# Performance work log

Measured on AMD Instinct MI355X. Metric: run time of the kernel, lower is better.

## Reference

```python
import jax, jax.numpy as jnp
import numpy as np

B, S, D = 4, 2048, 1024
P = 2
N_FEAT = 16          # n_feature_know
N_REST = 16          # n_restore_know
R = 128              # knowledge_rank
D_SPACE = 64


def setup_inputs() -> dict:
    key = jax.random.key(0)
    ks = jax.random.split(key, 6)
    x = jax.random.normal(ks[0], (B, S, D), dtype=jnp.float32)
    # per-token routing weights for each of P feature paths, in [0,1)
    feature_paths = jax.random.uniform(ks[1], (P, B, S, N_FEAT), dtype=jnp.float32)
    f_know = jax.random.normal(ks[2], (N_FEAT, D, R), dtype=jnp.float32) * 0.02
    r_know = jax.random.normal(ks[3], (N_REST, R, D), dtype=jnp.float32) * 0.02
    feature_emb = jax.random.normal(ks[4], (N_FEAT, D_SPACE), dtype=jnp.float32)
    W_router = jax.random.normal(ks[5], (D_SPACE + R, N_REST), dtype=jnp.float32) * 0.05
    return {"x": x, "feature_paths": feature_paths, "f_know": f_know,
            "r_know": r_know, "feature_emb": feature_emb, "W_router": W_router}


def reference(x, feature_paths, f_know, r_know, feature_emb, W_router):
    # Feature projection into all N low-rank banks: [B,S,N,R]
    all_h = jnp.einsum('bsd,ndr->bsnr', x, f_know)
    # Weighted sum over banks per path: [P,B,S,R]
    h_all = jnp.einsum('bsnr,pbsn->pbsr', all_h, feature_paths)
    # Context for restore routing: [P,B,S,D_SPACE]
    neuron_ctx = jnp.einsum('pbsn,nd->pbsd', feature_paths, feature_emb)
    # restore_input = cat([neuron_ctx, h]) -> router -> softmax restore weights
    restore_input = jnp.concatenate([neuron_ctx, h_all], axis=-1)  # [P,B,S,D_SPACE+R]
    logits = jnp.einsum('pbsc,cn->pbsn', restore_input, W_router)
    w = jax.nn.softmax(logits, axis=-1)                            # [P,B,S,N_REST]
    # Restore + per-token weighted combine, summed over P paths: [B,S,D]
    output = jnp.einsum('pbsr,nrd,pbsn->bsd', h_all, r_know, w)
    restore_aux_loss = jnp.float32(0.0)
    return output, restore_aux_loss
```

## Files before the change

kernel.cpp:

```cpp
#include <hip/hip_runtime.h>

typedef __attribute__((ext_vector_type(4))) float f32x4;
typedef __bf16 bf16x8 __attribute__((ext_vector_type(8)));
typedef unsigned short ushort_t;

#define T_TOK 8192
#define DIM   1024
#define NRCOL 2048

#define VMW(n)  asm volatile("s_waitcnt vmcnt(" #n ")" ::: "memory")
#define SB0()   __builtin_amdgcn_sched_barrier(0)
#define BAR()   __builtin_amdgcn_s_barrier()

static __device__ __forceinline__ unsigned short f2bf(float f) {
  unsigned int u = __builtin_bit_cast(unsigned int, f);
  u += 0x7fffu + ((u >> 16) & 1u);
  return (unsigned short)(u >> 16);
}
static __device__ __forceinline__ float bfbits2f(unsigned int lo16) {
  return __builtin_bit_cast(float, lo16 << 16);
}
static __device__ __forceinline__ void gload16(const void* g, void* l) {
  __builtin_amdgcn_global_load_lds((const __attribute__((address_space(1))) void*)g,
                                   (__attribute__((address_space(3))) void*)l, 16, 0, 0);
}

__global__ __launch_bounds__(256) void prep_kernel(const float* __restrict__ x,
                                                   const float* __restrict__ fk,
                                                   const float* __restrict__ rk,
                                                   unsigned short* __restrict__ Xbf,
                                                   unsigned short* __restrict__ W1t,
                                                   unsigned short* __restrict__ W2t) {
  const int bid = blockIdx.x, tid = threadIdx.x;
  if (bid < 2048) {
    const float4* in4 = (const float4*)x;
    uint2* o4 = (uint2*)Xbf;
    #pragma unroll
    for (int it = 0; it < 4; ++it) {
      const int i = bid * 256 + tid + it * 524288;
      float4 v = in4[i];
      uint2 o;
      o.x = (unsigned)f2bf(v.x) | ((unsigned)f2bf(v.y) << 16);
      o.y = (unsigned)f2bf(v.z) | ((unsigned)f2bf(v.w) << 16);
      o4[i] = o;
    }
    return;
  }
  __shared__ float tile[32][33];
  const float* src;
  unsigned short* dst;
  int rows, cols, r0, c0;
  if (bid < 4096) {
    const int b = bid - 2048;
    const int z = b >> 7, rem = b & 127;
    src = fk + (size_t)z * 1024 * 128;
    dst = W1t + (size_t)z * 128 * 1024;
    rows = 1024; cols = 128;
    c0 = (rem & 3) * 32; r0 = (rem >> 2) * 32;
  } else {
    const int b = bid - 4096;
    src = rk; dst = W2t;
    rows = 2048; cols = 1024;
    c0 = (b & 31) * 32; r0 = (b >> 5) * 32;
  }
  const int tx = tid & 31, ty = tid >> 5;
  #pragma unroll
  for (int i = 0; i < 32; i += 8)
    tile[ty + i][tx] = src[(size_t)(r0 + ty + i) * cols + c0 + tx];
  __syncthreads();
  #pragma unroll
  for (int i = 0; i < 32; i += 8)
    dst[(size_t)(c0 + ty + i) * rows + r0 + tx] = f2bf(tile[tx][ty + i]);
}

template<int BM, int BN, int K, bool OUT_BF16>
__global__ __launch_bounds__(256, 1) void gemmW(const ushort_t* __restrict__ A,
                                                const ushort_t* __restrict__ Bt,
                                                void* __restrict__ Cp, int N) {
  constexpr int nt = K / 64;
  constexpr int MF = BM / 32;
  constexpr int NF = BN / 32;
  constexpr int AR = BM / 32;
  constexpr int BR = BN / 32;
  __shared__ ushort_t As[3][BM * 64];
  __shared__ ushort_t Bs[3][BN * 64];

  const int tid = threadIdx.x;
  const int nx = gridDim.x;
  const int orig = blockIdx.y * nx + blockIdx.x;
  const int q = (nx * gridDim.y) >> 3;
  const int swz = (orig & 7) * q + (orig >> 3);
  const int bx = swz % nx, by = swz / nx;

  const int lane = tid & 63, wv = tid >> 6;
  const int wm = wv >> 1, wn = wv & 1;
  const int lrow = lane & 15, lk = lane >> 4;

  const ushort_t* Ab = A + (size_t)by * BM * K;
  const ushort_t* Bb = Bt + (size_t)bx * BN * K;

  const int srow = tid >> 3;
  const int sch = (tid & 7) ^ (srow & 7);
  const ushort_t* pA[AR];
  const ushort_t* pB[BR];
  #pragma unroll
  for (int r = 0; r < AR; ++r) pA[r] = Ab + (size_t)(r * 32 + srow) * K + sch * 8;
  #pragma unroll
  for (int r = 0; r < BR; ++r) pB[r] = Bb + (size_t)(r * 32 + srow) * K + sch * 8;
  const int dL = tid * 8;

  auto stage = [&](int s, int adv) {
    #pragma unroll
    for (int r = 0; r < AR; ++r) gload16(pA[r] + adv, (void*)&As[s][r * 2048 + dL]);
    #pragma unroll
    for (int r = 0; r < BR; ++r) gload16(pB[r] + adv, (void*)&Bs[s][r * 2048 + dL]);
  };

  int oA[MF], oB[NF];
  #pragma unroll
  for (int m = 0; m < MF; ++m) {
    const int r = wm * (BM / 2) + m * 16 + lrow;
    oA[m] = r * 64 + (lk ^ (r & 7)) * 8;
  }
  #pragma unroll
  for (int n = 0; n < NF; ++n) {
    const int r = wn * (BN / 2) + n * 16 + lrow;
    oB[n] = r * 64 + (lk ^ (r & 7)) * 8;
  }

  f32x4 acc[MF][NF];
  #pragma unroll
  for (int m = 0; m < MF; ++m)
    #pragma unroll
    for (int n = 0; n < NF; ++n)
      acc[m][n] = (f32x4){0.f, 0.f, 0.f, 0.f};

  stage(0, 0);
  stage(1, 64);
  VMW(12); SB0(); BAR(); SB0();

  #pragma unroll
  for (int t = 0; t < nt; ++t) {
    const int s = t % 3, s2 = (t + 2) % 3;
    if (t + 2 < nt) stage(s2, (t + 2) * 64);
    #pragma unroll
    for (int ks = 0; ks < 2; ++ks) {
      bf16x8 av[MF], bv[NF];
      #pragma unroll
      for (int m = 0; m < MF; ++m) av[m] = *(const bf16x8*)&As[s][oA[m] ^ (ks * 32)];
      #pragma unroll
      for (int n = 0; n < NF; ++n) bv[n] = *(const bf16x8*)&Bs[s][oB[n] ^ (ks * 32)];
      __builtin_amdgcn_s_setprio(1);
      #pragma unroll
      for (int m = 0; m < MF; ++m)
        #pragma unroll
        for (int n = 0; n < NF; ++n)
          acc[m][n] = __builtin_amdgcn_mfma_f32_16x16x32_bf16(av[m], bv[n], acc[m][n], 0, 0, 0);
      __builtin_amdgcn_s_setprio(0);
    }
    SB0();
    if (t + 2 < nt) { VMW(12); } else { VMW(0); }
    SB0(); BAR(); SB0();
  }

  #pragma unroll
  for (int m = 0; m < MF; ++m) {
    const int row0 = by * BM + wm * (BM / 2) + m * 16 + lk * 4;
    #pragma unroll
    for (int n = 0; n < NF; ++n) {
      const int col = bx * BN + wn * (BN / 2) + n * 16 + lrow;
      #pragma unroll
      for (int j = 0; j < 4; ++j) {
        const size_t idx = (size_t)(row0 + j) * N + col;
        if constexpr (OUT_BF16) ((ushort_t*)Cp)[idx] = f2bf(acc[m][n][j]);
        else                    ((float*)Cp)[idx] = acc[m][n][j];
      }
    }
  }
}

__global__ __launch_bounds__(256) void middle_kernel(const unsigned short* __restrict__ AH,
                                                     const float* __restrict__ fp,
                                                     const float* __restrict__ femb,
                                                     const float* __restrict__ Wr,
                                                     unsigned short* __restrict__ Mout,
                                                     float* __restrict__ auxout) {
  __shared__ float G[16][16];
  __shared__ float hs[4][2][128];
  __shared__ float wsm[4][2][16];
  const int tid = threadIdx.x;
  {
    const int n = tid >> 4, j = tid & 15;
    float s = 0.f;
    #pragma unroll
    for (int ds = 0; ds < 64; ++ds) s += femb[n * 64 + ds] * Wr[ds * 16 + j];
    G[n][j] = s;
  }
  const int wv = tid >> 6, l = tid & 63;
  const int t = blockIdx.x * 4 + wv;

  float p0[16], p1[16];
  #pragma unroll
  for (int n = 0; n < 16; ++n) {
    p0[n] = fp[t * 16 + n];
    p1[n] = fp[T_TOK * 16 + t * 16 + n];
  }

  float h00 = 0.f, h01 = 0.f, h10 = 0.f, h11 = 0.f;
  const unsigned short* ahrow = AH + (size_t)t * NRCOL;
  #pragma unroll
  for (int n = 0; n < 16; ++n) {
    const unsigned int v = *(const unsigned int*)(ahrow + n * 128 + 2 * l);
    const float a0 = bfbits2f(v & 0xffffu);
    const float a1 = bfbits2f(v >> 16);
    h00 += a0 * p0[n]; h01 += a1 * p0[n];
    h10 += a0 * p1[n]; h11 += a1 * p1[n];
  }
  hs[wv][0][2 * l] = h00; hs[wv][0][2 * l + 1] = h01;
  hs[wv][1][2 * l] = h10; hs[wv][1][2 * l + 1] = h11;
  __syncthreads();

  if (l < 32) {
    const int p = l >> 4, j = l & 15;
    float s = 0.f;
    #pragma unroll
    for (int n = 0; n < 16; ++n) s += (p ? p1[n] : p0[n]) * G[n][j];
    const float* hp = hs[wv][p];
    const float* wr = Wr + 64 * 16 + j;
    float s0 = 0.f, s1 = 0.f, s2 = 0.f, s3 = 0.f;
    #pragma unroll
    for (int r = 0; r < 128; r += 4) {
      s0 += hp[r]     * wr[(r)     * 16];
      s1 += hp[r + 1] * wr[(r + 1) * 16];
      s2 += hp[r + 2] * wr[(r + 2) * 16];
      s3 += hp[r + 3] * wr[(r + 3) * 16];
    }
    s += (s0 + s1) + (s2 + s3);
    float mx = s;
    #pragma unroll
    for (int d = 1; d < 16; d <<= 1) mx = fmaxf(mx, __shfl_xor(mx, d, 64));
    const float e = __expf(s - mx);
    float sum = e;
    #pragma unroll
    for (int d = 1; d < 16; d <<= 1) sum += __shfl_xor(sum, d, 64);
    wsm[wv][p][j] = e / sum;
  }
  __syncthreads();

  unsigned short* mrow = Mout + (size_t)t * NRCOL;
  #pragma unroll
  for (int n = 0; n < 16; ++n) {
    const float w0 = wsm[wv][0][n], w1 = wsm[wv][1][n];
    const float m0 = w0 * h00 + w1 * h10;
    const float m1 = w0 * h01 + w1 * h11;
    const unsigned int pk = (unsigned)f2bf(m0) | ((unsigned)f2bf(m1) << 16);
    *(unsigned int*)(mrow + n * 128 + 2 * l) = pk;
  }
  if (blockIdx.x == 0 && tid == 0) auxout[0] = 0.f;
}

extern "C" void kernel_launch(void* const* d_in, const int* in_sizes, int n_in,
                              void* d_out, int out_size, void* d_ws, size_t ws_size,
                              hipStream_t stream) {
  const float* x    = (const float*)d_in[0];
  const float* fp   = (const float*)d_in[1];
  const float* fk   = (const float*)d_in[2];
  const float* rk   = (const float*)d_in[3];
  const float* femb = (const float*)d_in[4];
  const float* Wr   = (const float*)d_in[5];
  float* out = (float*)d_out;

  char* ws = (char*)d_ws;
  unsigned short* Xbf = (unsigned short*)ws;
  unsigned short* W1t = (unsigned short*)(ws + 16u * 1024 * 1024);
  unsigned short* Mb  = (unsigned short*)ws;
  unsigned short* W2t = (unsigned short*)(ws + 32u * 1024 * 1024);
  unsigned short* AH  = (unsigned short*)(ws + 36u * 1024 * 1024);

  prep_kernel<<<6144, 256, 0, stream>>>(x, fk, rk, Xbf, W1t, W2t);
  gemmW<256, 128, 1024, true><<<dim3(NRCOL / 128, T_TOK / 256), 256, 0, stream>>>(Xbf, W1t, AH, NRCOL);
  middle_kernel<<<T_TOK / 4, 256, 0, stream>>>(AH, fp, femb, Wr, Mb, out + 8388608);
  gemmW<128, 256, 2048, false><<<dim3(DIM / 256, T_TOK / 128), 256, 0, stream>>>(Mb, W2t, out, DIM);
}
```

Before: 127.2 us.

## Use 128x128 double-buffered GEMM tiles with 2 blocks/CU; parallelize router dot

Replaces the templated triple-buffered GEMM, which used 256x128 or 128x256 tiles at one block per CU, with a fixed 128x128 tile, double-buffered kernel launched at two blocks per CU. This roughly doubles the grid and allows more resident waves to hide memory latency, at the cost of less operand reuse per tile and a shallower prefetch pipeline. The middle kernel now stages the router weight slice in shared memory and splits the 128-long router dot product across all 64 lanes with a shuffle reduction, instead of leaving half the lanes idle.

```diff
diff --git a/kernel.cpp b/kernel.cpp
--- a/kernel.cpp
+++ b/kernel.cpp
@@ -73,17 +73,13 @@
     dst[(size_t)(c0 + ty + i) * rows + r0 + tx] = f2bf(tile[tx][ty + i]);
 }
 
-template<int BM, int BN, int K, bool OUT_BF16>
-__global__ __launch_bounds__(256, 1) void gemmW(const ushort_t* __restrict__ A,
+template<int K, bool OUT_BF16>
+__global__ __launch_bounds__(256, 2) void gemmD(const ushort_t* __restrict__ A,
                                                 const ushort_t* __restrict__ Bt,
                                                 void* __restrict__ Cp, int N) {
   constexpr int nt = K / 64;
-  constexpr int MF = BM / 32;
-  constexpr int NF = BN / 32;
-  constexpr int AR = BM / 32;
-  constexpr int BR = BN / 32;
-  __shared__ ushort_t As[3][BM * 64];
-  __shared__ ushort_t Bs[3][BN * 64];
+  __shared__ ushort_t As[2][128 * 64];
+  __shared__ ushort_t Bs[2][128 * 64];
 
   const int tid = threadIdx.x;
   const int nx = gridDim.x;
@@ -96,79 +92,79 @@
   const int wm = wv >> 1, wn = wv & 1;
   const int lrow = lane & 15, lk = lane >> 4;
 
-  const ushort_t* Ab = A + (size_t)by * BM * K;
-  const ushort_t* Bb = Bt + (size_t)bx * BN * K;
+  const ushort_t* Ab = A + (size_t)by * 128 * K;
+  const ushort_t* Bb = Bt + (size_t)bx * 128 * K;
 
   const int srow = tid >> 3;
   const int sch = (tid & 7) ^ (srow & 7);
-  const ushort_t* pA[AR];
-  const ushort_t* pB[BR];
-  #pragma unroll
-  for (int r = 0; r < AR; ++r) pA[r] = Ab + (size_t)(r * 32 + srow) * K + sch * 8;
-  #pragma unroll
-  for (int r = 0; r < BR; ++r) pB[r] = Bb + (size_t)(r * 32 + srow) * K + sch * 8;
+  const ushort_t* pA[4];
+  const ushort_t* pB[4];
+  #pragma unroll
+  for (int r = 0; r < 4; ++r) {
+    pA[r] = Ab + (size_t)(r * 32 + srow) * K + sch * 8;
+    pB[r] = Bb + (size_t)(r * 32 + srow) * K + sch * 8;
+  }
   const int dL = tid * 8;
 
   auto stage = [&](int s, int adv) {
     #pragma unroll
-    for (int r = 0; r < AR; ++r) gload16(pA[r] + adv, (void*)&As[s][r * 2048 + dL]);
-    #pragma unroll
-    for (int r = 0; r < BR; ++r) gload16(pB[r] + adv, (void*)&Bs[s][r * 2048 + dL]);
+    for (int r = 0; r < 4; ++r) gload16(pA[r] + adv, (void*)&As[s][r * 2048 + dL]);
+    #pragma unroll
+    for (int r = 0; r < 4; ++r) gload16(pB[r] + adv, (void*)&Bs[s][r * 2048 + dL]);
   };
 
-  int oA[MF], oB[NF];
-  #pragma unroll
-  for (int m = 0; m < MF; ++m) {
-    const int r = wm * (BM / 2) + m * 16 + lrow;
+  int oA[4], oB[4];
+  #pragma unroll
+  for (int m = 0; m < 4; ++m) {
+    const int r = wm * 64 + m * 16 + lrow;
     oA[m] = r * 64 + (lk ^ (r & 7)) * 8;
   }
   #pragma unroll
-  for (int n = 0; n < NF; ++n) {
-    const int r = wn * (BN / 2) + n * 16 + lrow;
+  for (int n = 0; n < 4; ++n) {
+    const int r = wn * 64 + n * 16 + lrow;
     oB[n] = r * 64 + (lk ^ (r & 7)) * 8;
   }
 
-  f32x4 acc[MF][NF];
-  #pragma unroll
-  for (int m = 0; m < MF; ++m)
-    #pragma unroll
-    for (int n = 0; n < NF; ++n)
+  f32x4 acc[4][4];
+  #pragma unroll
+  for (int m = 0; m < 4; ++m)
+    #pragma unroll
+    for (int n = 0; n < 4; ++n)
       acc[m][n] = (f32x4){0.f, 0.f, 0.f, 0.f};
 
   stage(0, 0);
-  stage(1, 64);
-  VMW(12); SB0(); BAR(); SB0();
+  VMW(0); SB0(); BAR(); SB0();
 
   #pragma unroll
   for (int t = 0; t < nt; ++t) {
-    const int s = t % 3, s2 = (t + 2) % 3;
-    if (t + 2 < nt) stage(s2, (t + 2) * 64);
+    const int s = t & 1;
+    if (t + 1 < nt) stage(s ^ 1, (t + 1) * 64);
     #pragma unroll
     for (int ks = 0; ks < 2; ++ks) {
-      bf16x8 av[MF], bv[NF];
-      #pragma unroll
-      for (int m = 0; m < MF; ++m) av[m] = *(const bf16x8*)&As[s][oA[m] ^ (ks * 32)];
-      #pragma unroll
-      for (int n = 0; n < NF; ++n) bv[n] = *(const bf16x8*)&Bs[s][oB[n] ^ (ks * 32)];
+      bf16x8 av[4], bv[4];
+      #pragma unroll
+      for (int m = 0; m < 4; ++m) av[m] = *(const bf16x8*)&As[s][oA[m] ^ (ks * 32)];
+      #pragma unroll
+      for (int n = 0; n < 4; ++n) bv[n] = *(const bf16x8*)&Bs[s][oB[n] ^ (ks * 32)];
       __builtin_amdgcn_s_setprio(1);
       #pragma unroll
-      for (int m = 0; m < MF; ++m)
+      for (int m = 0; m < 4; ++m)
         #pragma unroll
-        for (int n = 0; n < NF; ++n)
+        for (int n = 0; n < 4; ++n)
           acc[m][n] = __builtin_amdgcn_mfma_f32_16x16x32_bf16(av[m], bv[n], acc[m][n], 0, 0, 0);
       __builtin_amdgcn_s_setprio(0);
     }
     SB0();
-    if (t + 2 < nt) { VMW(12); } else { VMW(0); }
-    SB0(); BAR(); SB0();
-  }
-
-  #pragma unroll
-  for (int m = 0; m < MF; ++m) {
-    const int row0 = by * BM + wm * (BM / 2) + m * 16 + lk * 4;
-    #pragma unroll
-    for (int n = 0; n < NF; ++n) {
-      const int col = bx * BN + wn * (BN / 2) + n * 16 + lrow;
+    if (t + 1 < nt) VMW(0);
+    BAR(); SB0();
+  }
+
+  #pragma unroll
+  for (int m = 0; m < 4; ++m) {
+    const int row0 = by * 128 + wm * 64 + m * 16 + lk * 4;
+    #pragma unroll
+    for (int n = 0; n < 4; ++n) {
+      const int col = bx * 128 + wn * 64 + n * 16 + lrow;
       #pragma unroll
       for (int j = 0; j < 4; ++j) {
         const size_t idx = (size_t)(row0 + j) * N + col;
@@ -186,6 +182,7 @@
                                                      unsigned short* __restrict__ Mout,
                                                      float* __restrict__ auxout) {
   __shared__ float G[16][16];
+  __shared__ float WrBs[128 * 16];
   __shared__ float hs[4][2][128];
   __shared__ float wsm[4][2][16];
   const int tid = threadIdx.x;
@@ -195,6 +192,9 @@
     #pragma unroll
     for (int ds = 0; ds < 64; ++ds) s += femb[n * 64 + ds] * Wr[ds * 16 + j];
     G[n][j] = s;
+    #pragma unroll
+    for (int k = 0; k < 8; ++k)
+      WrBs[tid * 8 + k] = Wr[64 * 16 + tid * 8 + k];
   }
   const int wv = tid >> 6, l = tid & 63;
   const int t = blockIdx.x * 4 + wv;
@@ -220,22 +220,25 @@
   hs[wv][1][2 * l] = h10; hs[wv][1][2 * l + 1] = h11;
   __syncthreads();
 
-  if (l < 32) {
-    const int p = l >> 4, j = l & 15;
-    float s = 0.f;
-    #pragma unroll
-    for (int n = 0; n < 16; ++n) s += (p ? p1[n] : p0[n]) * G[n][j];
-    const float* hp = hs[wv][p];
-    const float* wr = Wr + 64 * 16 + j;
+  {
+    const int p = l >> 5, seg = (l >> 4) & 1, j = l & 15;
+    const float* hp = hs[wv][p] + seg * 64;
+    const float* wb = WrBs + seg * 64 * 16 + j;
     float s0 = 0.f, s1 = 0.f, s2 = 0.f, s3 = 0.f;
     #pragma unroll
-    for (int r = 0; r < 128; r += 4) {
-      s0 += hp[r]     * wr[(r)     * 16];
-      s1 += hp[r + 1] * wr[(r + 1) * 16];
-      s2 += hp[r + 2] * wr[(r + 2) * 16];
-      s3 += hp[r + 3] * wr[(r + 3) * 16];
-    }
-    s += (s0 + s1) + (s2 + s3);
+    for (int r = 0; r < 64; r += 4) {
+      s0 += hp[r]     * wb[(r)     * 16];
+      s1 += hp[r + 1] * wb[(r + 1) * 16];
+      s2 += hp[r + 2] * wb[(r + 2) * 16];
+      s3 += hp[r + 3] * wb[(r + 3) * 16];
+    }
+    float s = (s0 + s1) + (s2 + s3);
+    s += __shfl_xor(s, 16, 64);
+    #pragma unroll
+    for (int n = 0; n < 16; ++n) {
+      const float fv = p ? p1[n] : p0[n];
+      s += fv * G[n][j];
+    }
     float mx = s;
     #pragma unroll
     for (int d = 1; d < 16; d <<= 1) mx = fmaxf(mx, __shfl_xor(mx, d, 64));
@@ -243,7 +246,7 @@
     float sum = e;
     #pragma unroll
     for (int d = 1; d < 16; d <<= 1) sum += __shfl_xor(sum, d, 64);
-    wsm[wv][p][j] = e / sum;
+    if (seg == 0) wsm[wv][p][j] = e / sum;
   }
   __syncthreads();
 
@@ -278,7 +281,7 @@
   unsigned short* AH  = (unsigned short*)(ws + 36u * 1024 * 1024);
 
   prep_kernel<<<6144, 256, 0, stream>>>(x, fk, rk, Xbf, W1t, W2t);
-  gemmW<256, 128, 1024, true><<<dim3(NRCOL / 128, T_TOK / 256), 256, 0, stream>>>(Xbf, W1t, AH, NRCOL);
+  gemmD<1024, true><<<dim3(NRCOL / 128, T_TOK / 128), 256, 0, stream>>>(Xbf, W1t, AH, NRCOL);
   middle_kernel<<<T_TOK / 4, 256, 0, stream>>>(AH, fp, femb, Wr, Mb, out + 8388608);
-  gemmW<128, 256, 2048, false><<<dim3(DIM / 256, T_TOK / 128), 256, 0, stream>>>(Mb, W2t, out, DIM);
-}
+  gemmD<2048, false><<<dim3(DIM / 128, T_TOK / 128), 256, 0, stream>>>(Mb, W2t, out, DIM);
+}
```

Result: faster. 107.7 us, median of 3 (-15.4%).
